# Optimization experiments

Hardware: AMD Instinct MI355X
Metric: run time of the kernel (lower is better)

## Reference

```python
import jax, jax.numpy as jnp
import numpy as np

B, S, E, D, DV = 4, 4096, 1024, 64, 1024
NEG_INF = jnp.inf


def setup_inputs() -> dict:
    key = jax.random.key(0)
    ks = jax.random.split(key, 5)
    x = jax.random.normal(ks[0], (B, S, E), dtype=jnp.float32)
    Wq = jax.random.normal(ks[1], (E, D), dtype=jnp.float32) * 0.02
    Wk = jax.random.normal(ks[2], (E, D), dtype=jnp.float32) * 0.02
    Wv = jax.random.normal(ks[3], (E, DV), dtype=jnp.float32) * 0.02
    bq = jnp.zeros((D,), dtype=jnp.float32)
    bk = jnp.zeros((D,), dtype=jnp.float32)
    bv = jnp.zeros((DV,), dtype=jnp.float32)
    pad = jax.random.uniform(ks[4], (B, S)) > 0.9
    mask_padding_x = jnp.where(pad, -jnp.inf, 0.0).astype(jnp.float32)
    return {"x": x, "Wq": Wq, "bq": bq, "Wk": Wk, "bk": bk,
            "Wv": Wv, "bv": bv, "mask_padding_x": mask_padding_x}


def _padding_mask(mask_padding_x):
    # Faithful replication of the torch mask-combination logic (self-attn: y mask == x mask).
    mask_x = mask_padding_x[:, :, None]   # [B, Sx, 1]
    mask_y = mask_padding_x[:, None, :]   # [B, 1, Sy]
    # (-inf)*(-inf)=+inf kept; 0*(-inf)=nan -> 0
    prod = jnp.nan_to_num(mask_x * mask_y, nan=0.0, posinf=jnp.inf)
    # one side padded -> -inf; both padded -> inf + (-inf) + (-inf) = nan -> 0; both valid -> 0
    final = jnp.nan_to_num(prod + mask_y + mask_x, nan=0.0, posinf=0.0, neginf=-jnp.inf)
    return final  # [B, Sx, Sy]


def _causal_mask(n):
    # create_mask: strictly-upper-triangular -inf, zeros on/below diagonal
    return jnp.triu(jnp.full((n, n), -jnp.inf, dtype=jnp.float32), k=1)


def reference(x, Wq, bq, Wk, bk, Wv, bv, mask_padding_x):
    # self-attention path (y = x), mask=True (causal), dropout in eval mode (identity)
    Q = jnp.einsum('bse,ed->bsd', x, Wq) + bq          # [B,S,D]
    K = jnp.einsum('bse,ed->bsd', x, Wk) + bk          # [B,S,D]
    V = jnp.einsum('bse,ev->bsv', x, Wv) + bv          # [B,S,DV]
    scale = 1.0 / jnp.sqrt(jnp.float32(D))
    QK = jnp.einsum('bqd,bkd->bqk', Q, K) * scale      # [B,S,S]
    QK = QK + _padding_mask(mask_padding_x)
    QK = QK + _causal_mask(x.shape[1])
    attn = jax.nn.softmax(QK, axis=-1)
    return jnp.einsum('bqk,bkv->bqv', attn, V)         # [B,S,DV]
```

## Files before the change

### kernel.cpp

```cpp
#include <hip/hip_runtime.h>
#include <stdint.h>

typedef __attribute__((ext_vector_type(8))) short short8;
typedef __attribute__((ext_vector_type(4))) float floatx4;

__device__ __forceinline__ unsigned short f2bf(float f) {
    unsigned u = __float_as_uint(f);
    u += 0x7FFFu + ((u >> 16) & 1u);
    return (unsigned short)(u >> 16);
}

__device__ __forceinline__ void gload_lds16(const void* g, void* l) {
    __builtin_amdgcn_global_load_lds(
        (const __attribute__((address_space(1))) unsigned int*)g,
        (__attribute__((address_space(3))) unsigned int*)l, 16, 0, 0);
}

__global__ __launch_bounds__(256)
void conv_x(const float* __restrict__ x, unsigned short* __restrict__ xb) {
    const size_t total = (size_t)16384 * 1024;
    for (size_t i = ((size_t)blockIdx.x * 256 + threadIdx.x) * 8; i < total;
         i += (size_t)2048 * 256 * 8) {
        float4 a = *(const float4*)&x[i];
        float4 b = *(const float4*)&x[i + 4];
        uint4 o;
        o.x = f2bf(a.x) | ((unsigned)f2bf(a.y) << 16);
        o.y = f2bf(a.z) | ((unsigned)f2bf(a.w) << 16);
        o.z = f2bf(b.x) | ((unsigned)f2bf(b.y) << 16);
        o.w = f2bf(b.z) | ((unsigned)f2bf(b.w) << 16);
        *(uint4*)&xb[i] = o;
    }
}

__global__ __launch_bounds__(256)
void transpose_all(const float* __restrict__ Wv, const float* __restrict__ Wq,
                   const float* __restrict__ Wk, unsigned short* __restrict__ Wt) {
    __shared__ float T[64][65];
    const int t = threadIdx.x;
    const int k0 = blockIdx.x * 64;
    const int y = blockIdx.y;
    const float* src; int N, n0, rowoff;
    if (y < 16)      { src = Wv; N = 1024; n0 = y * 64; rowoff = 0; }
    else if (y == 16){ src = Wq; N = 64;   n0 = 0;      rowoff = 1024; }
    else             { src = Wk; N = 64;   n0 = 0;      rowoff = 1088; }
    const int r = t >> 4, c4 = (t & 15) * 4;
#pragma unroll
    for (int i = 0; i < 4; i++) {
        float4 v = *(const float4*)&src[(size_t)(k0 + r + 16 * i) * N + n0 + c4];
        T[r + 16 * i][c4] = v.x; T[r + 16 * i][c4 + 1] = v.y;
        T[r + 16 * i][c4 + 2] = v.z; T[r + 16 * i][c4 + 3] = v.w;
    }
    __syncthreads();
#pragma unroll
    for (int i = 0; i < 4; i++) {
        const int n = rowoff + n0 + r + 16 * i;
        unsigned short b0 = f2bf(T[c4 + 0][r + 16 * i]);
        unsigned short b1 = f2bf(T[c4 + 1][r + 16 * i]);
        unsigned short b2 = f2bf(T[c4 + 2][r + 16 * i]);
        unsigned short b3 = f2bf(T[c4 + 3][r + 16 * i]);
        uint2 pv;
        pv.x = b0 | ((unsigned)b1 << 16);
        pv.y = b2 | ((unsigned)b3 << 16);
        *(uint2*)&Wt[(size_t)n * 1024 + k0 + c4] = pv;
    }
}

__global__ __launch_bounds__(576)
void pack_bias_all(const float* __restrict__ bv, const float* __restrict__ bq,
                   const float* __restrict__ bk, float* __restrict__ bf) {
    const int t = blockIdx.x * 576 + threadIdx.x;
    if (t < 1024) bf[t] = bv[t];
    else if (t < 1088) bf[t] = bq[t - 1024];
    else if (t < 1152) bf[t] = bk[t - 1088];
}

__global__ __launch_bounds__(256)
void gemm_fused(const unsigned short* __restrict__ A,
                const unsigned short* __restrict__ Bt,
                const float* __restrict__ bias,
                unsigned short* __restrict__ Vt,
                unsigned short* __restrict__ QKb)
{
    __shared__ unsigned short As[128 * 32];
    __shared__ unsigned short Bs[128 * 32];
    const int tid = threadIdx.x;
    const int w = tid >> 6, l = tid & 63;
    const int quad = l >> 4, l16 = l & 15;
    const int wr = w >> 1, wc = w & 1;
    const int m0 = blockIdx.x * 128, n0 = blockIdx.y * 128;

    const int lr = l >> 2, lk = (l & 3) * 8;
    const unsigned short* Ag0 = A + (size_t)(m0 + w * 16 + lr) * 1024 + lk;
    const unsigned short* Ag1 = Ag0 + (size_t)64 * 1024;
    const unsigned short* Bg0 = Bt + (size_t)(n0 + w * 16 + lr) * 1024 + lk;
    const unsigned short* Bg1 = Bg0 + (size_t)64 * 1024;
    unsigned short* Al0 = &As[w * 512 + l * 8];
    unsigned short* Bl0 = &Bs[w * 512 + l * 8];

    floatx4 acc[4][4];
#pragma unroll
    for (int i = 0; i < 4; i++)
#pragma unroll
        for (int j = 0; j < 4; j++) acc[i][j] = (floatx4)0.f;

    for (int e0 = 0; e0 < 1024; e0 += 32) {
        gload_lds16(Ag0 + e0, Al0);
        gload_lds16(Ag1 + e0, Al0 + 2048);
        gload_lds16(Bg0 + e0, Bl0);
        gload_lds16(Bg1 + e0, Bl0 + 2048);
        __syncthreads();
        short8 af[4], bf[4];
#pragma unroll
        for (int i = 0; i < 4; i++)
            af[i] = *(const short8*)&As[(wr * 64 + i * 16 + l16) * 32 + quad * 8];
#pragma unroll
        for (int j = 0; j < 4; j++)
            bf[j] = *(const short8*)&Bs[(wc * 64 + j * 16 + l16) * 32 + quad * 8];
#pragma unroll
        for (int i = 0; i < 4; i++)
#pragma unroll
            for (int j = 0; j < 4; j++)
                acc[i][j] = __builtin_amdgcn_mfma_f32_16x16x32_bf16(af[i], bf[j], acc[i][j], 0, 0, 0);
        __syncthreads();
    }

    const bool toQK = (n0 >= 1024);
#pragma unroll
    for (int j = 0; j < 4; j++) {
        const int n = n0 + wc * 64 + j * 16 + l16;
        const float bn = bias[n];
#pragma unroll
        for (int i = 0; i < 4; i++) {
            const int mb = m0 + wr * 64 + i * 16 + quad * 4;
            if (!toQK) {
                unsigned short t[4];
#pragma unroll
                for (int r = 0; r < 4; r++) t[r] = f2bf(acc[i][j][r] + bn);
                uint2 pv;
                pv.x = t[0] | ((unsigned)t[1] << 16);
                pv.y = t[2] | ((unsigned)t[3] << 16);
                *(uint2*)&Vt[(size_t)n * 16384 + mb] = pv;
            } else {
#pragma unroll
                for (int r = 0; r < 4; r++)
                    QKb[(size_t)(mb + r) * 128 + (n - 1024)] = f2bf(acc[i][j][r] + bn);
            }
        }
    }
}

__global__ __launch_bounds__(512, 4)
void attn_fused(const unsigned short* __restrict__ QKb,
                const unsigned short* __restrict__ Vt,
                const float* __restrict__ maskx,
                float* __restrict__ out)
{
    __shared__ unsigned short Qs[64 * 72];
    __shared__ unsigned short Ps[2][64 * 40];
    __shared__ float Ls[64];

    const int tid = threadIdx.x;
    const int wave = tid >> 6, lane = tid & 63;
    const int quad = lane >> 4, l16 = lane & 15;
    const int bid = blockIdx.x;
    const int dvh = bid & 1;
    const int b = (bid >> 1) & 3;
    const int t = bid >> 3;
    const int qt = (t < 32) ? (63 - t) : (t - 32);
    const int q0 = qt * 64;
    const int gq0 = b * 4096 + q0;

    if (tid < 64) Ls[tid] = 0.f;
    {
        const int r = tid >> 3, c = (tid & 7) * 8;
        uint4 v = *(const uint4*)&QKb[(size_t)(gq0 + r) * 128 + c];
        *(uint4*)&Qs[r * 72 + c] = v;
    }
    __syncthreads();

    const int rb = wave >> 1;
    const int kb = wave & 1;
    bool pq[4];
#pragma unroll
    for (int r = 0; r < 4; r++)
        pq[r] = maskx[b * 4096 + q0 + rb * 16 + quad * 4 + r] < -1e30f;

    const short8 qa0 = *(const short8*)&Qs[(rb * 16 + l16) * 72 + quad * 8];
    const short8 qa1 = *(const short8*)&Qs[(rb * 16 + l16) * 72 + 32 + quad * 8];

    floatx4 acc[4][4];
#pragma unroll
    for (int i = 0; i < 4; i++)
#pragma unroll
        for (int j = 0; j < 4; j++) acc[i][j] = (floatx4)0.f;
    float lacc[4] = {0.f, 0.f, 0.f, 0.f};

    const int niter = 2 * qt + 2;
    const float scale = 0.125f;
    const int dv0 = dvh * 512 + wave * 64;

    const unsigned short* kptr = QKb + ((size_t)(b * 4096 + kb * 16 + l16) * 128 + 64 + quad * 8);
    const float* mptr = maskx + b * 4096 + kb * 16 + l16;
    size_t voff[4];
#pragma unroll
    for (int cb = 0; cb < 4; cb++)
        voff[cb] = (size_t)(dv0 + cb * 16 + l16) * 16384 + b * 4096 + quad * 8;

    short8 kc0 = *(const short8*)kptr;
    short8 kc1 = *(const short8*)(kptr + 32);
    float mval = *mptr;
    short8 vb[4];
#pragma unroll
    for (int cb = 0; cb < 4; cb++)
        vb[cb] = *(const short8*)&Vt[voff[cb]];

    for (int kt = 0; kt < niter; kt++) {
        const int k0 = kt * 32;
        floatx4 s = (floatx4)0.f;
        s = __builtin_amdgcn_mfma_f32_16x16x32_bf16(qa0, kc0, s, 0, 0, 0);
        s = __builtin_amdgcn_mfma_f32_16x16x32_bf16(qa1, kc1, s, 0, 0, 0);
        const bool pk = mval < -1e30f;
        {
            int kn = k0 + 32 + kb * 16 + l16;
            if (kn > 4095) kn = 4095;
            const unsigned short* np = QKb + ((size_t)(b * 4096 + kn) * 128 + 64 + quad * 8);
            kc0 = *(const short8*)np;
            kc1 = *(const short8*)(np + 32);
            mval = maskx[b * 4096 + kn];
        }
        const int kg = k0 + kb * 16 + l16;
        unsigned short pbits[4];
#pragma unroll
        for (int r = 0; r < 4; r++) {
            const int qrow = q0 + rb * 16 + quad * 4 + r;
            float p = 0.f;
            if (kg <= qrow && pk == pq[r]) p = __expf(s[r] * scale);
            lacc[r] += p;
            pbits[r] = f2bf(p);
        }
        unsigned short* Pw = Ps[kt & 1];
#pragma unroll
        for (int r = 0; r < 4; r++)
            Pw[(rb * 16 + quad * 4 + r) * 40 + kb * 16 + l16] = pbits[r];
        asm volatile("s_waitcnt lgkmcnt(0)" ::: "memory");
        __builtin_amdgcn_s_barrier();
        __builtin_amdgcn_sched_barrier(0);
        const unsigned short* Pr = Ps[kt & 1];
        short8 pa[4];
#pragma unroll
        for (int r2 = 0; r2 < 4; r2++)
            pa[r2] = *(const short8*)&Pr[(r2 * 16 + l16) * 40 + quad * 8];
#pragma unroll
        for (int cb = 0; cb < 4; cb++)
#pragma unroll
            for (int r2 = 0; r2 < 4; r2++)
                acc[r2][cb] = __builtin_amdgcn_mfma_f32_16x16x32_bf16(pa[r2], vb[cb], acc[r2][cb], 0, 0, 0);
        {
            const int kv = (k0 + 32 > 4064) ? 4064 : (k0 + 32);
#pragma unroll
            for (int cb = 0; cb < 4; cb++)
                vb[cb] = *(const short8*)&Vt[voff[cb] + kv];
        }
    }

#pragma unroll
    for (int r = 0; r < 4; r++) {
        float v = lacc[r];
        v += __shfl_xor(v, 1);
        v += __shfl_xor(v, 2);
        v += __shfl_xor(v, 4);
        v += __shfl_xor(v, 8);
        if (l16 == 0) atomicAdd(&Ls[rb * 16 + quad * 4 + r], v);
    }
    __syncthreads();

#pragma unroll
    for (int r2 = 0; r2 < 4; r2++) {
#pragma unroll
        for (int r = 0; r < 4; r++) {
            const int qrow = q0 + r2 * 16 + quad * 4 + r;
            const float inv = 1.f / Ls[r2 * 16 + quad * 4 + r];
#pragma unroll
            for (int cb = 0; cb < 4; cb++)
                out[(size_t)(b * 4096 + qrow) * 1024 + dv0 + cb * 16 + l16] = acc[r2][cb][r] * inv;
        }
    }
}

extern "C" void kernel_launch(void* const* d_in, const int* in_sizes, int n_in,
                              void* d_out, int out_size, void* d_ws, size_t ws_size,
                              hipStream_t stream) {
    const float* x  = (const float*)d_in[0];
    const float* Wq = (const float*)d_in[1];
    const float* bq = (const float*)d_in[2];
    const float* Wk = (const float*)d_in[3];
    const float* bk = (const float*)d_in[4];
    const float* Wv = (const float*)d_in[5];
    const float* bv = (const float*)d_in[6];
    const float* mk = (const float*)d_in[7];
    float* out = (float*)d_out;

    char* ws = (char*)d_ws;
    unsigned short* Xb   = (unsigned short*)ws;
    unsigned short* Vt   = (unsigned short*)(ws + (33554432));
    unsigned short* Wt   = (unsigned short*)(ws + (67108864));
    unsigned short* QKb  = (unsigned short*)(ws + (69468160));
    float*          bfull= (float*)(ws + (73662464));

    conv_x<<<2048, 256, 0, stream>>>(x, Xb);
    transpose_all<<<dim3(16, 18), 256, 0, stream>>>(Wv, Wq, Wk, Wt);
    pack_bias_all<<<2, 576, 0, stream>>>(bv, bq, bk, bfull);

    gemm_fused<<<dim3(128, 9), 256, 0, stream>>>(Xb, Wt, bfull, Vt, QKb);

    attn_fused<<<dim3(4 * 64 * 2), 512, 0, stream>>>(QKb, Vt, mk, out);
}
```

Measured before the change: 394.1 us.

## Software-pipeline QK scores one tile ahead of the PV MFMA accumulation

Adds a prologue that computes the first tile's probabilities. The loop body then runs the PV MFMAs for tile kt and the QK MFMAs for tile kt+1 back to back, followed by the exp and mask work and the LDS write for kt+1. This is meant to overlap softmax VALU work with matrix work and to hide LDS and global load latency. It also raises wave priority with s_setprio around the MFMA block. In exchange it makes the loop-carried dependences more complex and may raise register pressure.

```diff
diff --git a/kernel.cpp b/kernel.cpp
--- a/kernel.cpp
+++ b/kernel.cpp
@@ -199,68 +199,84 @@
     const float scale = 0.125f;
     const int dv0 = dvh * 512 + wave * 64;
 
-    const unsigned short* kptr = QKb + ((size_t)(b * 4096 + kb * 16 + l16) * 128 + 64 + quad * 8);
-    const float* mptr = maskx + b * 4096 + kb * 16 + l16;
     size_t voff[4];
 #pragma unroll
     for (int cb = 0; cb < 4; cb++)
         voff[cb] = (size_t)(dv0 + cb * 16 + l16) * 16384 + b * 4096 + quad * 8;
 
-    short8 kc0 = *(const short8*)kptr;
-    short8 kc1 = *(const short8*)(kptr + 32);
-    float mval = *mptr;
     short8 vb[4];
 #pragma unroll
     for (int cb = 0; cb < 4; cb++)
         vb[cb] = *(const short8*)&Vt[voff[cb]];
-
-    for (int kt = 0; kt < niter; kt++) {
-        const int k0 = kt * 32;
+    {
+        const unsigned short* kp = QKb + ((size_t)(b * 4096 + kb * 16 + l16) * 128 + 64 + quad * 8);
+        const short8 kc0 = *(const short8*)kp;
+        const short8 kc1 = *(const short8*)(kp + 32);
+        const float mv = maskx[b * 4096 + kb * 16 + l16];
         floatx4 s = (floatx4)0.f;
         s = __builtin_amdgcn_mfma_f32_16x16x32_bf16(qa0, kc0, s, 0, 0, 0);
         s = __builtin_amdgcn_mfma_f32_16x16x32_bf16(qa1, kc1, s, 0, 0, 0);
-        const bool pk = mval < -1e30f;
+        const bool pk = mv < -1e30f;
+        const int kg = kb * 16 + l16;
+        unsigned short* Pw = Ps[0];
+#pragma unroll
+        for (int r = 0; r < 4; r++) {
+            const int qrow = q0 + rb * 16 + quad * 4 + r;
+            float p = 0.f;
+            if (kg <= qrow && pk == pq[r]) p = __expf(s[r] * scale);
+            lacc[r] += p;
+            Pw[(rb * 16 + quad * 4 + r) * 40 + kb * 16 + l16] = f2bf(p);
+        }
+    }
+    asm volatile("s_waitcnt lgkmcnt(0)" ::: "memory");
+    __builtin_amdgcn_s_barrier();
+    __builtin_amdgcn_sched_barrier(0);
+
+    for (int kt = 0; kt < niter; kt++) {
+        const int k0 = kt * 32;
+        short8 kc0, kc1;
+        float mvn;
         {
             int kn = k0 + 32 + kb * 16 + l16;
             if (kn > 4095) kn = 4095;
             const unsigned short* np = QKb + ((size_t)(b * 4096 + kn) * 128 + 64 + quad * 8);
             kc0 = *(const short8*)np;
             kc1 = *(const short8*)(np + 32);
-            mval = maskx[b * 4096 + kn];
-        }
-        const int kg = k0 + kb * 16 + l16;
-        unsigned short pbits[4];
+            mvn = maskx[b * 4096 + kn];
+        }
+        const unsigned short* Pr = Ps[kt & 1];
+        __builtin_amdgcn_s_setprio(1);
+#pragma unroll
+        for (int r2 = 0; r2 < 4; r2++) {
+            const short8 pa = *(const short8*)&Pr[(r2 * 16 + l16) * 40 + quad * 8];
+#pragma unroll
+            for (int cb = 0; cb < 4; cb++)
+                acc[r2][cb] = __builtin_amdgcn_mfma_f32_16x16x32_bf16(pa, vb[cb], acc[r2][cb], 0, 0, 0);
+        }
+        floatx4 s = (floatx4)0.f;
+        s = __builtin_amdgcn_mfma_f32_16x16x32_bf16(qa0, kc0, s, 0, 0, 0);
+        s = __builtin_amdgcn_mfma_f32_16x16x32_bf16(qa1, kc1, s, 0, 0, 0);
+        __builtin_amdgcn_s_setprio(0);
+        {
+            const int kv = (k0 + 32 > 4064) ? 4064 : (k0 + 32);
+#pragma unroll
+            for (int cb = 0; cb < 4; cb++)
+                vb[cb] = *(const short8*)&Vt[voff[cb] + kv];
+        }
+        const bool pk = mvn < -1e30f;
+        const int kg = k0 + 32 + kb * 16 + l16;
+        unsigned short* Pw = Ps[(kt + 1) & 1];
 #pragma unroll
         for (int r = 0; r < 4; r++) {
             const int qrow = q0 + rb * 16 + quad * 4 + r;
             float p = 0.f;
             if (kg <= qrow && pk == pq[r]) p = __expf(s[r] * scale);
             lacc[r] += p;
-            pbits[r] = f2bf(p);
-        }
-        unsigned short* Pw = Ps[kt & 1];
-#pragma unroll
-        for (int r = 0; r < 4; r++)
-            Pw[(rb * 16 + quad * 4 + r) * 40 + kb * 16 + l16] = pbits[r];
+            Pw[(rb * 16 + quad * 4 + r) * 40 + kb * 16 + l16] = f2bf(p);
+        }
         asm volatile("s_waitcnt lgkmcnt(0)" ::: "memory");
         __builtin_amdgcn_s_barrier();
         __builtin_amdgcn_sched_barrier(0);
-        const unsigned short* Pr = Ps[kt & 1];
-        short8 pa[4];
-#pragma unroll
-        for (int r2 = 0; r2 < 4; r2++)
-            pa[r2] = *(const short8*)&Pr[(r2 * 16 + l16) * 40 + quad * 8];
-#pragma unroll
-        for (int cb = 0; cb < 4; cb++)
-#pragma unroll
-            for (int r2 = 0; r2 < 4; r2++)
-                acc[r2][cb] = __builtin_amdgcn_mfma_f32_16x16x32_bf16(pa[r2], vb[cb], acc[r2][cb], 0, 0, 0);
-        {
-            const int kv = (k0 + 32 > 4064) ? 4064 : (k0 + 32);
-#pragma unroll
-            for (int cb = 0; cb < 4; cb++)
-                vb[cb] = *(const short8*)&Vt[voff[cb] + kv];
-        }
     }
 
 #pragma unroll
```

Result: faster. 362.6 us (-8.0%).
